# Kernel tuning notes

Measured on AMD Instinct MI355X. Metric: run time of the kernel, lower is better.

Reference implementation:

```python
import jax, jax.numpy as jnp
import numpy as np

COMMITMENT_COST = 0.25
NUM_EMBEDDINGS = 4096
EMBEDDING_DIM = 64


def setup_inputs() -> dict:
    key = jax.random.key(0)
    k1, k2 = jax.random.split(key)
    inputs = jax.random.normal(k1, (32, 32, 32, EMBEDDING_DIM), dtype=jnp.float32)
    # torch init: uniform(-1/K, 1/K)
    lim = 1.0 / NUM_EMBEDDINGS
    embeddings = jax.random.uniform(k2, (NUM_EMBEDDINGS, EMBEDDING_DIM),
                                    dtype=jnp.float32, minval=-lim, maxval=lim)
    return {"inputs": inputs, "embeddings": embeddings}


def reference(inputs, embeddings):
    input_shape = inputs.shape
    flat = inputs.reshape(-1, EMBEDDING_DIM)                      # [N, D]
    x_sq = jnp.sum(flat * flat, axis=1, keepdims=True)            # [N, 1]
    e_sq = jnp.sum(embeddings * embeddings, axis=1)               # [K]
    distances = x_sq - 2.0 * (flat @ embeddings.T) + e_sq[None, :]  # [N, K]
    encoding_indices = jnp.argmin(distances, axis=1)              # [N]
    quantized = embeddings[encoding_indices].reshape(input_shape)  # direct gather == one-hot matmul
    e_latent_loss = jnp.mean((jax.lax.stop_gradient(quantized) - inputs) ** 2)
    q_latent_loss = jnp.mean((quantized - jax.lax.stop_gradient(inputs)) ** 2)
    loss = q_latent_loss + COMMITMENT_COST * e_latent_loss
    # straight-through estimator
    quantized_st = inputs + jax.lax.stop_gradient(quantized - inputs)
    return quantized_st, loss, encoding_indices[:, None]
```

## Files before the change

kernel.cpp:

```cpp
#include <hip/hip_runtime.h>


#define NROWS 32768
#define NK 4096
#define ND 64
#define LOSS_OFF 2097152u
#define IDX_OFF  2097153u
#define EMAX 2.44140625e-4f
#define CAP 48

typedef __attribute__((ext_vector_type(8))) short bf16x8;
typedef __attribute__((ext_vector_type(16))) float f32x16;

__device__ __forceinline__ short f2bf(float f) {
  union { float f; unsigned u; } v; v.f = f;
  unsigned u = v.u;
  return (short)((u + 0x7fffu + ((u >> 16) & 1u)) >> 16);
}
__device__ __forceinline__ unsigned fmap(float f) {
  unsigned u = __float_as_uint(f);
  return (u & 0x80000000u) ? ~u : (u | 0x80000000u);
}
__device__ __forceinline__ float funmap(unsigned m) {
  return __uint_as_float((m & 0x80000000u) ? (m & 0x7fffffffu) : ~m);
}

__global__ __launch_bounds__(256) void k_prep(
    const float* __restrict__ xg, const float* __restrict__ emb,
    bf16x8* __restrict__ ebfT, bf16x8* __restrict__ xbfF,
    float* __restrict__ xsqA, float* __restrict__ marg,
    int* __restrict__ cnt, unsigned* __restrict__ rowbest,
    double* __restrict__ acc) {
  int rt = blockIdx.x, tid = threadIdx.x, l = tid & 63;
  int row = rt * 32 + (l & 31);
  int d0 = (tid >> 6) * 16 + ((l >> 5) << 3);
  {
    const float4* p = reinterpret_cast<const float4*>(xg + (size_t)row * ND + d0);
    float4 u = p[0], v = p[1];
    bf16x8 o;
    o[0] = f2bf(u.x); o[1] = f2bf(u.y); o[2] = f2bf(u.z); o[3] = f2bf(u.w);
    o[4] = f2bf(v.x); o[5] = f2bf(v.y); o[6] = f2bf(v.z); o[7] = f2bf(v.w);
    xbfF[rt * 256 + tid] = o;
  }
  if (rt < 128) {
    int code = rt * 32 + (l & 31);
    const float4* p = reinterpret_cast<const float4*>(emb + (size_t)code * ND + d0);
    float4 u = p[0], v = p[1];
    bf16x8 o;
    o[0] = f2bf(u.x); o[1] = f2bf(u.y); o[2] = f2bf(u.z); o[3] = f2bf(u.w);
    o[4] = f2bf(v.x); o[5] = f2bf(v.y); o[6] = f2bf(v.z); o[7] = f2bf(v.w);
    ebfT[rt * 256 + tid] = o;
  }
  if (tid < 32) {
    int r2 = rt * 32 + tid;
    const float4* xr = reinterpret_cast<const float4*>(xg + (size_t)r2 * ND);
    float xs = 0.f, S = 0.f;
#pragma unroll
    for (int j = 0; j < 16; ++j) {
      float4 w = xr[j];
      xs = fmaf(w.x, w.x, xs); xs = fmaf(w.y, w.y, xs);
      xs = fmaf(w.z, w.z, xs); xs = fmaf(w.w, w.w, xs);
      S += fabsf(w.x) + fabsf(w.y) + fabsf(w.z) + fabsf(w.w);
    }
    xsqA[r2] = xs;
    marg[r2] = EMAX * S * 0.015625f + 1e-5f;
    cnt[r2] = 0;
    rowbest[r2] = 0u;
  }
  if (rt == 0 && tid == 0) acc[0] = 0.0;
}

__global__ __launch_bounds__(512, 8) void k_scan(
    const bf16x8* __restrict__ ebfT, const bf16x8* __restrict__ xbfF,
    const float* __restrict__ marg, unsigned* __restrict__ rowbest,
    int* __restrict__ cnt, uint2* __restrict__ list) {
  __shared__ bf16x8 Alds[2048];
  int bid = blockIdx.x;
  int rb = bid >> 4, cg = bid & 15;
  int tid = threadIdx.x, wv = tid >> 6, l = tid & 63;
  int rt = rb * 8 + wv;
  const bf16x8* xf = xbfF + rt * 256;
  bf16x8 b0 = xf[l], b1 = xf[64 + l], b2 = xf[128 + l], b3 = xf[192 + l];
  const bf16x8* src = ebfT + cg * 2048;
#pragma unroll
  for (int it = 0; it < 4; ++it) Alds[it * 512 + tid] = src[it * 512 + tid];
  __syncthreads();

  int row = rt * 32 + (l & 31);
  float mg = marg[row];
  float tmax[8];
#pragma unroll
  for (int tt = 0; tt < 8; ++tt) {
    bf16x8 a0 = Alds[tt * 256 + l],       a1 = Alds[tt * 256 + 64 + l],
           a2 = Alds[tt * 256 + 128 + l], a3 = Alds[tt * 256 + 192 + l];
    f32x16 acc;
#pragma unroll
    for (int r = 0; r < 16; ++r) acc[r] = 0.f;
    acc = __builtin_amdgcn_mfma_f32_32x32x16_bf16(a0, b0, acc, 0, 0, 0);
    acc = __builtin_amdgcn_mfma_f32_32x32x16_bf16(a1, b1, acc, 0, 0, 0);
    acc = __builtin_amdgcn_mfma_f32_32x32x16_bf16(a2, b2, acc, 0, 0, 0);
    acc = __builtin_amdgcn_mfma_f32_32x32x16_bf16(a3, b3, acc, 0, 0, 0);
    float m = fmaxf(fmaxf(fmaxf(acc[0], acc[1]), fmaxf(acc[2], acc[3])),
                    fmaxf(fmaxf(acc[4], acc[5]), fmaxf(acc[6], acc[7])));
    float m2 = fmaxf(fmaxf(fmaxf(acc[8], acc[9]), fmaxf(acc[10], acc[11])),
                     fmaxf(fmaxf(acc[12], acc[13]), fmaxf(acc[14], acc[15])));
    tmax[tt] = fmaxf(m, m2);
  }
  float rm = tmax[0];
#pragma unroll
  for (int tt = 1; tt < 8; ++tt) rm = fmaxf(rm, tmax[tt]);
  rm = fmaxf(rm, __shfl_xor(rm, 32, 64));
  atomicMax(&rowbest[row], fmap(rm));
  __syncthreads();
  float g = funmap(atomicMax(&rowbest[row], 0u));
  float thr = g - mg;
#pragma unroll
  for (int tt = 0; tt < 8; ++tt) {
    if (__any(tmax[tt] >= thr)) {
      bf16x8 a0 = Alds[tt * 256 + l],       a1 = Alds[tt * 256 + 64 + l],
             a2 = Alds[tt * 256 + 128 + l], a3 = Alds[tt * 256 + 192 + l];
      f32x16 acc;
#pragma unroll
      for (int r = 0; r < 16; ++r) acc[r] = 0.f;
      acc = __builtin_amdgcn_mfma_f32_32x32x16_bf16(a0, b0, acc, 0, 0, 0);
      acc = __builtin_amdgcn_mfma_f32_32x32x16_bf16(a1, b1, acc, 0, 0, 0);
      acc = __builtin_amdgcn_mfma_f32_32x32x16_bf16(a2, b2, acc, 0, 0, 0);
      acc = __builtin_amdgcn_mfma_f32_32x32x16_bf16(a3, b3, acc, 0, 0, 0);
      int kb = cg * 256 + tt * 32 + ((l >> 5) << 2);
#pragma unroll
      for (int r = 0; r < 16; ++r) {
        if (acc[r] >= thr) {
          int k = kb + (r & 3) + ((r >> 2) << 3);
          int slot = atomicAdd(&cnt[row], 1);
          if (slot < CAP)
            list[(size_t)row * CAP + slot] =
                make_uint2((unsigned)k, __float_as_uint(acc[r]));
        }
      }
    }
  }
}

__global__ __launch_bounds__(128) void k_pickout(
    const float* __restrict__ xg, const float* __restrict__ emb,
    const int* __restrict__ cnt, const uint2* __restrict__ list,
    const float* __restrict__ marg, const float* __restrict__ xsqA,
    float* __restrict__ out, double* __restrict__ acc) {
  int row = blockIdx.x * 128 + threadIdx.x;
  int mylane = threadIdx.x & 63;
  float4 X[16];
  const float4* xr = reinterpret_cast<const float4*>(xg + (size_t)row * ND);
#pragma unroll
  for (int j = 0; j < 16; ++j) X[j] = xr[j];
  float xs = xsqA[row], mg = marg[row];
  int c = cnt[row];
  unsigned long long best = ~0ull;

  int cc = c < CAP ? c : CAP;
  const uint2* L = list + (size_t)row * CAP;
  float m = -3.0e38f;
  for (int i = 0; i < cc; ++i) m = fmaxf(m, __uint_as_float(L[i].y));
  float thr = m - mg;
  for (int i = 0; i < cc; ++i) {
    uint2 e = L[i];
    if (__uint_as_float(e.y) >= thr) {
      int k = (int)e.x;
      const float4* er = reinterpret_cast<const float4*>(emb + (size_t)k * ND);
      float q0 = 0.f, q1 = 0.f, q2 = 0.f, q3 = 0.f;
#pragma unroll
      for (int j = 0; j < 16; ++j) {
        float4 E = er[j];
        q0 = fmaf(X[j].x, E.x, q0); q1 = fmaf(X[j].y, E.y, q1);
        q2 = fmaf(X[j].z, E.z, q2); q3 = fmaf(X[j].w, E.w, q3);
      }
      float dot = (q0 + q1) + (q2 + q3);
      float dist = xs - 2.0f * dot;
      unsigned long long key =
          ((unsigned long long)__float_as_uint(dist) << 32) | (unsigned)k;
      best = best < key ? best : key;
    }
  }

  unsigned long long ovf = __ballot(c > CAP);
  while (ovf) {
    int srcl = __ffsll(ovf) - 1;
    ovf &= ovf - 1;
    int orow = __shfl(row, srcl, 64);
    float ys = __shfl(xs, srcl, 64);
    float4 Y[16];
    const float4* yr = reinterpret_cast<const float4*>(xg + (size_t)orow * ND);
#pragma unroll
    for (int j = 0; j < 16; ++j) Y[j] = yr[j];
    unsigned long long wb = ~0ull;
    for (int i = 0; i < 64; ++i) {
      int k = mylane * 64 + i;
      const float4* er = reinterpret_cast<const float4*>(emb + (size_t)k * ND);
      float q0 = 0.f, q1 = 0.f, q2 = 0.f, q3 = 0.f;
#pragma unroll
      for (int j = 0; j < 16; ++j) {
        float4 E = er[j];
        q0 = fmaf(Y[j].x, E.x, q0); q1 = fmaf(Y[j].y, E.y, q1);
        q2 = fmaf(Y[j].z, E.z, q2); q3 = fmaf(Y[j].w, E.w, q3);
      }
      float dot = (q0 + q1) + (q2 + q3);
      float dist = ys - 2.0f * dot;
      unsigned long long key =
          ((unsigned long long)__float_as_uint(dist) << 32) | (unsigned)k;
      wb = wb < key ? wb : key;
    }
#pragma unroll
    for (int off = 32; off > 0; off >>= 1) {
      unsigned long long o = __shfl_xor(wb, off, 64);
      wb = wb < o ? wb : o;
    }
    if (mylane == srcl) best = wb;
  }

  unsigned kwin = ((unsigned)(best & 0xffffffffull)) & 4095u;
  const float4* er = reinterpret_cast<const float4*>(emb + (size_t)kwin * ND);
  float4* op = reinterpret_cast<float4*>(out + (size_t)row * ND);
  float s2 = 0.f;
#pragma unroll
  for (int j = 0; j < 16; ++j) {
    float4 E = er[j];
    float d0 = E.x - X[j].x, d1 = E.y - X[j].y;
    float d2 = E.z - X[j].z, d3 = E.w - X[j].w;
    float4 O = {X[j].x + d0, X[j].y + d1, X[j].z + d2, X[j].w + d3};
    op[j] = O;
    s2 += d0 * d0 + d1 * d1 + d2 * d2 + d3 * d3;
  }
  out[IDX_OFF + (unsigned)row] = (float)kwin;
  double s = (double)s2;
#pragma unroll
  for (int off = 32; off > 0; off >>= 1) s += __shfl_down(s, off, 64);
  if (mylane == 0) atomicAdd(acc, s);
}

__global__ void k_fin(const double* __restrict__ acc, float* __restrict__ out) {
  if (threadIdx.x == 0) out[LOSS_OFF] = (float)(1.25 * acc[0] / 2097152.0);
}

extern "C" void kernel_launch(void* const* d_in, const int* in_sizes, int n_in,
                              void* d_out, int out_size, void* d_ws, size_t ws_size,
                              hipStream_t stream) {
  const float* xg = (const float*)d_in[0];
  const float* emb = (const float*)d_in[1];
  float* out = (float*)d_out;
  char* w = (char*)d_ws;
  bf16x8* ebfT = (bf16x8*)w;
  bf16x8* xbfF = (bf16x8*)(w + 524288);
  float* xsqA = (float*)(w + 4718592);
  float* marg = (float*)(w + 4849664);
  int* cnt    = (int*)(w + 4980736);
  unsigned* rowbest = (unsigned*)(w + 5111808);
  double* acc = (double*)(w + 5373952);
  uint2* list = (uint2*)(w + 5373968);

  k_prep<<<1024, 256, 0, stream>>>(xg, emb, ebfT, xbfF, xsqA, marg, cnt, rowbest, acc);
  k_scan<<<2048, 512, 0, stream>>>(ebfT, xbfF, marg, rowbest, cnt, list);
  k_pickout<<<256, 128, 0, stream>>>(xg, emb, cnt, list, marg, xsqA, out, acc);
  k_fin<<<1, 64, 0, stream>>>(acc, out);
}
```

Before: 131.8 us.

## Single-pass scan with running-max threshold, double-buffered codebook, 8-lane pickout

The two-pass scan, which did a global atomicMax over each row's best score and then recomputed the MFMA tiles, is replaced by a single pass. Each block streams a quarter of the codebook through double-buffered LDS and emits candidates against a per-block running-max threshold. This removes the rowbest buffer, the atomics and the duplicated MFMA work. The pickout kernel now spreads each row over 8 lanes and computes ||x||^2 inline instead of reading it from prep. The running threshold is looser early in the scan, so more candidates may be emitted and rows may overflow CAP more often, which triggers the costly brute-force fallback.

```diff
diff --git a/kernel.cpp b/kernel.cpp
--- a/kernel.cpp
+++ b/kernel.cpp
@@ -17,20 +17,11 @@
   unsigned u = v.u;
   return (short)((u + 0x7fffu + ((u >> 16) & 1u)) >> 16);
 }
-__device__ __forceinline__ unsigned fmap(float f) {
-  unsigned u = __float_as_uint(f);
-  return (u & 0x80000000u) ? ~u : (u | 0x80000000u);
-}
-__device__ __forceinline__ float funmap(unsigned m) {
-  return __uint_as_float((m & 0x80000000u) ? (m & 0x7fffffffu) : ~m);
-}
 
 __global__ __launch_bounds__(256) void k_prep(
     const float* __restrict__ xg, const float* __restrict__ emb,
     bf16x8* __restrict__ ebfT, bf16x8* __restrict__ xbfF,
-    float* __restrict__ xsqA, float* __restrict__ marg,
-    int* __restrict__ cnt, unsigned* __restrict__ rowbest,
-    double* __restrict__ acc) {
+    float* __restrict__ marg, int* __restrict__ cnt, double* __restrict__ acc) {
   int rt = blockIdx.x, tid = threadIdx.x, l = tid & 63;
   int row = rt * 32 + (l & 31);
   int d0 = (tid >> 6) * 16 + ((l >> 5) << 3);
@@ -54,158 +45,159 @@
   if (tid < 32) {
     int r2 = rt * 32 + tid;
     const float4* xr = reinterpret_cast<const float4*>(xg + (size_t)r2 * ND);
-    float xs = 0.f, S = 0.f;
+    float S = 0.f;
 #pragma unroll
     for (int j = 0; j < 16; ++j) {
       float4 w = xr[j];
-      xs = fmaf(w.x, w.x, xs); xs = fmaf(w.y, w.y, xs);
-      xs = fmaf(w.z, w.z, xs); xs = fmaf(w.w, w.w, xs);
       S += fabsf(w.x) + fabsf(w.y) + fabsf(w.z) + fabsf(w.w);
     }
-    xsqA[r2] = xs;
     marg[r2] = EMAX * S * 0.015625f + 1e-5f;
     cnt[r2] = 0;
-    rowbest[r2] = 0u;
   }
   if (rt == 0 && tid == 0) acc[0] = 0.0;
 }
 
-__global__ __launch_bounds__(512, 8) void k_scan(
+__global__ __launch_bounds__(256, 4) void k_scan(
     const bf16x8* __restrict__ ebfT, const bf16x8* __restrict__ xbfF,
-    const float* __restrict__ marg, unsigned* __restrict__ rowbest,
-    int* __restrict__ cnt, uint2* __restrict__ list) {
-  __shared__ bf16x8 Alds[2048];
+    const float* __restrict__ marg, int* __restrict__ cnt,
+    uint2* __restrict__ list) {
+  __shared__ bf16x8 Alds[2][1024];
   int bid = blockIdx.x;
-  int rb = bid >> 4, cg = bid & 15;
+  int rg = bid >> 2, q = bid & 3;
   int tid = threadIdx.x, wv = tid >> 6, l = tid & 63;
-  int rt = rb * 8 + wv;
+  int rt = rg * 4 + wv;
+  int row = rt * 32 + (l & 31);
   const bf16x8* xf = xbfF + rt * 256;
   bf16x8 b0 = xf[l], b1 = xf[64 + l], b2 = xf[128 + l], b3 = xf[192 + l];
-  const bf16x8* src = ebfT + cg * 2048;
-#pragma unroll
-  for (int it = 0; it < 4; ++it) Alds[it * 512 + tid] = src[it * 512 + tid];
+  float mg = marg[row];
+  const bf16x8* src = ebfT + q * 8192;
+
+#pragma unroll
+  for (int it = 0; it < 4; ++it) Alds[0][it * 256 + tid] = src[it * 256 + tid];
   __syncthreads();
 
-  int row = rt * 32 + (l & 31);
-  float mg = marg[row];
-  float tmax[8];
-#pragma unroll
-  for (int tt = 0; tt < 8; ++tt) {
-    bf16x8 a0 = Alds[tt * 256 + l],       a1 = Alds[tt * 256 + 64 + l],
-           a2 = Alds[tt * 256 + 128 + l], a3 = Alds[tt * 256 + 192 + l];
-    f32x16 acc;
-#pragma unroll
-    for (int r = 0; r < 16; ++r) acc[r] = 0.f;
-    acc = __builtin_amdgcn_mfma_f32_32x32x16_bf16(a0, b0, acc, 0, 0, 0);
-    acc = __builtin_amdgcn_mfma_f32_32x32x16_bf16(a1, b1, acc, 0, 0, 0);
-    acc = __builtin_amdgcn_mfma_f32_32x32x16_bf16(a2, b2, acc, 0, 0, 0);
-    acc = __builtin_amdgcn_mfma_f32_32x32x16_bf16(a3, b3, acc, 0, 0, 0);
-    float m = fmaxf(fmaxf(fmaxf(acc[0], acc[1]), fmaxf(acc[2], acc[3])),
-                    fmaxf(fmaxf(acc[4], acc[5]), fmaxf(acc[6], acc[7])));
-    float m2 = fmaxf(fmaxf(fmaxf(acc[8], acc[9]), fmaxf(acc[10], acc[11])),
-                     fmaxf(fmaxf(acc[12], acc[13]), fmaxf(acc[14], acc[15])));
-    tmax[tt] = fmaxf(m, m2);
-  }
-  float rm = tmax[0];
-#pragma unroll
-  for (int tt = 1; tt < 8; ++tt) rm = fmaxf(rm, tmax[tt]);
-  rm = fmaxf(rm, __shfl_xor(rm, 32, 64));
-  atomicMax(&rowbest[row], fmap(rm));
-  __syncthreads();
-  float g = funmap(atomicMax(&rowbest[row], 0u));
-  float thr = g - mg;
-#pragma unroll
-  for (int tt = 0; tt < 8; ++tt) {
-    if (__any(tmax[tt] >= thr)) {
-      bf16x8 a0 = Alds[tt * 256 + l],       a1 = Alds[tt * 256 + 64 + l],
-             a2 = Alds[tt * 256 + 128 + l], a3 = Alds[tt * 256 + 192 + l];
-      f32x16 acc;
-#pragma unroll
-      for (int r = 0; r < 16; ++r) acc[r] = 0.f;
-      acc = __builtin_amdgcn_mfma_f32_32x32x16_bf16(a0, b0, acc, 0, 0, 0);
-      acc = __builtin_amdgcn_mfma_f32_32x32x16_bf16(a1, b1, acc, 0, 0, 0);
-      acc = __builtin_amdgcn_mfma_f32_32x32x16_bf16(a2, b2, acc, 0, 0, 0);
-      acc = __builtin_amdgcn_mfma_f32_32x32x16_bf16(a3, b3, acc, 0, 0, 0);
-      int kb = cg * 256 + tt * 32 + ((l >> 5) << 2);
-#pragma unroll
-      for (int r = 0; r < 16; ++r) {
-        if (acc[r] >= thr) {
-          int k = kb + (r & 3) + ((r >> 2) << 3);
-          int slot = atomicAdd(&cnt[row], 1);
-          if (slot < CAP)
-            list[(size_t)row * CAP + slot] =
-                make_uint2((unsigned)k, __float_as_uint(acc[r]));
+  float rm = -3.0e38f;
+  for (int ch = 0; ch < 8; ++ch) {
+    int cur = ch & 1;
+    bf16x8 p0, p1, p2, p3;
+    if (ch < 7) {
+      const bf16x8* s2 = src + (ch + 1) * 1024;
+      p0 = s2[tid]; p1 = s2[256 + tid]; p2 = s2[512 + tid]; p3 = s2[768 + tid];
+    }
+#pragma unroll
+    for (int tt = 0; tt < 4; ++tt) {
+      const bf16x8* A = &Alds[cur][tt * 256];
+      bf16x8 a0 = A[l], a1 = A[64 + l], a2 = A[128 + l], a3 = A[192 + l];
+      f32x16 ac;
+#pragma unroll
+      for (int r = 0; r < 16; ++r) ac[r] = 0.f;
+      ac = __builtin_amdgcn_mfma_f32_32x32x16_bf16(a0, b0, ac, 0, 0, 0);
+      ac = __builtin_amdgcn_mfma_f32_32x32x16_bf16(a1, b1, ac, 0, 0, 0);
+      ac = __builtin_amdgcn_mfma_f32_32x32x16_bf16(a2, b2, ac, 0, 0, 0);
+      ac = __builtin_amdgcn_mfma_f32_32x32x16_bf16(a3, b3, ac, 0, 0, 0);
+      float m = fmaxf(fmaxf(fmaxf(ac[0], ac[1]), fmaxf(ac[2], ac[3])),
+                      fmaxf(fmaxf(ac[4], ac[5]), fmaxf(ac[6], ac[7])));
+      float m2 = fmaxf(fmaxf(fmaxf(ac[8], ac[9]), fmaxf(ac[10], ac[11])),
+                       fmaxf(fmaxf(ac[12], ac[13]), fmaxf(ac[14], ac[15])));
+      m = fmaxf(m, m2);
+      m = fmaxf(m, __shfl_xor(m, 32, 64));
+      rm = fmaxf(rm, m);
+      float thr = rm - mg;
+      if (__any(m >= thr)) {
+        int kb = q * 1024 + ch * 128 + tt * 32 + ((l >> 5) << 2);
+#pragma unroll
+        for (int r = 0; r < 16; ++r) {
+          if (ac[r] >= thr) {
+            int k = kb + (r & 3) + ((r >> 2) << 3);
+            int slot = atomicAdd(&cnt[row], 1);
+            if (slot < CAP)
+              list[(size_t)row * CAP + slot] =
+                  make_uint2((unsigned)k, __float_as_uint(ac[r]));
+          }
         }
       }
     }
-  }
-}
-
-__global__ __launch_bounds__(128) void k_pickout(
+    if (ch < 7) {
+      bf16x8* D = &Alds[cur ^ 1][0];
+      D[tid] = p0; D[256 + tid] = p1; D[512 + tid] = p2; D[768 + tid] = p3;
+    }
+    __syncthreads();
+  }
+}
+
+__global__ __launch_bounds__(256, 4) void k_pickout(
     const float* __restrict__ xg, const float* __restrict__ emb,
     const int* __restrict__ cnt, const uint2* __restrict__ list,
-    const float* __restrict__ marg, const float* __restrict__ xsqA,
-    float* __restrict__ out, double* __restrict__ acc) {
-  int row = blockIdx.x * 128 + threadIdx.x;
-  int mylane = threadIdx.x & 63;
+    const float* __restrict__ marg, float* __restrict__ out,
+    double* __restrict__ acc) {
+  int tid = threadIdx.x, mylane = tid & 63, wv = tid >> 6;
+  int g = mylane >> 3, j = mylane & 7;
+  int row = blockIdx.x * 32 + wv * 8 + g;
+  const float4* xr = reinterpret_cast<const float4*>(xg + (size_t)row * ND);
   float4 X[16];
-  const float4* xr = reinterpret_cast<const float4*>(xg + (size_t)row * ND);
-#pragma unroll
-  for (int j = 0; j < 16; ++j) X[j] = xr[j];
-  float xs = xsqA[row], mg = marg[row];
+#pragma unroll
+  for (int i = 0; i < 16; ++i) X[i] = xr[i];
+  float xs = 0.f;
+#pragma unroll
+  for (int i = 0; i < 16; ++i) {
+    xs = fmaf(X[i].x, X[i].x, xs); xs = fmaf(X[i].y, X[i].y, xs);
+    xs = fmaf(X[i].z, X[i].z, xs); xs = fmaf(X[i].w, X[i].w, xs);
+  }
+  float mg = marg[row];
   int c = cnt[row];
-  unsigned long long best = ~0ull;
-
   int cc = c < CAP ? c : CAP;
   const uint2* L = list + (size_t)row * CAP;
   float m = -3.0e38f;
-  for (int i = 0; i < cc; ++i) m = fmaxf(m, __uint_as_float(L[i].y));
+  for (int i = j; i < cc; i += 8) m = fmaxf(m, __uint_as_float(L[i].y));
+#pragma unroll
+  for (int off = 4; off > 0; off >>= 1) m = fmaxf(m, __shfl_xor(m, off, 8));
   float thr = m - mg;
-  for (int i = 0; i < cc; ++i) {
+  unsigned long long best = ~0ull;
+  for (int i = j; i < cc; i += 8) {
     uint2 e = L[i];
     if (__uint_as_float(e.y) >= thr) {
-      int k = (int)e.x;
-      const float4* er = reinterpret_cast<const float4*>(emb + (size_t)k * ND);
+      const float4* er = reinterpret_cast<const float4*>(emb + ((size_t)e.x << 6));
       float q0 = 0.f, q1 = 0.f, q2 = 0.f, q3 = 0.f;
 #pragma unroll
-      for (int j = 0; j < 16; ++j) {
-        float4 E = er[j];
-        q0 = fmaf(X[j].x, E.x, q0); q1 = fmaf(X[j].y, E.y, q1);
-        q2 = fmaf(X[j].z, E.z, q2); q3 = fmaf(X[j].w, E.w, q3);
+      for (int t = 0; t < 16; ++t) {
+        float4 E = er[t];
+        q0 = fmaf(X[t].x, E.x, q0); q1 = fmaf(X[t].y, E.y, q1);
+        q2 = fmaf(X[t].z, E.z, q2); q3 = fmaf(X[t].w, E.w, q3);
       }
       float dot = (q0 + q1) + (q2 + q3);
       float dist = xs - 2.0f * dot;
       unsigned long long key =
-          ((unsigned long long)__float_as_uint(dist) << 32) | (unsigned)k;
+          ((unsigned long long)__float_as_uint(dist) << 32) | (unsigned long long)e.x;
       best = best < key ? best : key;
     }
   }
-
-  unsigned long long ovf = __ballot(c > CAP);
+#pragma unroll
+  for (int off = 4; off > 0; off >>= 1) {
+    unsigned long long o = __shfl_xor(best, off, 8);
+    best = best < o ? best : o;
+  }
+  unsigned long long ovf = __ballot(j == 0 && c > CAP);
   while (ovf) {
     int srcl = __ffsll(ovf) - 1;
     ovf &= ovf - 1;
     int orow = __shfl(row, srcl, 64);
     float ys = __shfl(xs, srcl, 64);
-    float4 Y[16];
     const float4* yr = reinterpret_cast<const float4*>(xg + (size_t)orow * ND);
-#pragma unroll
-    for (int j = 0; j < 16; ++j) Y[j] = yr[j];
     unsigned long long wb = ~0ull;
     for (int i = 0; i < 64; ++i) {
       int k = mylane * 64 + i;
-      const float4* er = reinterpret_cast<const float4*>(emb + (size_t)k * ND);
+      const float4* er = reinterpret_cast<const float4*>(emb + ((size_t)k << 6));
       float q0 = 0.f, q1 = 0.f, q2 = 0.f, q3 = 0.f;
 #pragma unroll
-      for (int j = 0; j < 16; ++j) {
-        float4 E = er[j];
-        q0 = fmaf(Y[j].x, E.x, q0); q1 = fmaf(Y[j].y, E.y, q1);
-        q2 = fmaf(Y[j].z, E.z, q2); q3 = fmaf(Y[j].w, E.w, q3);
+      for (int t = 0; t < 16; ++t) {
+        float4 Y = yr[t]; float4 E = er[t];
+        q0 = fmaf(Y.x, E.x, q0); q1 = fmaf(Y.y, E.y, q1);
+        q2 = fmaf(Y.z, E.z, q2); q3 = fmaf(Y.w, E.w, q3);
       }
       float dot = (q0 + q1) + (q2 + q3);
       float dist = ys - 2.0f * dot;
       unsigned long long key =
-          ((unsigned long long)__float_as_uint(dist) << 32) | (unsigned)k;
+          ((unsigned long long)__float_as_uint(dist) << 32) | (unsigned long long)k;
       wb = wb < key ? wb : key;
     }
 #pragma unroll
@@ -213,23 +205,21 @@
       unsigned long long o = __shfl_xor(wb, off, 64);
       wb = wb < o ? wb : o;
     }
-    if (mylane == srcl) best = wb;
-  }
-
+    if ((mylane >> 3) == (srcl >> 3)) best = wb;
+  }
   unsigned kwin = ((unsigned)(best & 0xffffffffull)) & 4095u;
-  const float4* er = reinterpret_cast<const float4*>(emb + (size_t)kwin * ND);
+  const float4* er = reinterpret_cast<const float4*>(emb + ((size_t)kwin << 6));
+  float4 E0 = er[2 * j], E1 = er[2 * j + 1];
+  float4 X0 = X[2 * j], X1 = X[2 * j + 1];
+  float d0 = E0.x - X0.x, d1 = E0.y - X0.y, d2 = E0.z - X0.z, d3 = E0.w - X0.w;
+  float d4 = E1.x - X1.x, d5 = E1.y - X1.y, d6 = E1.z - X1.z, d7 = E1.w - X1.w;
+  float4 O0 = {X0.x + d0, X0.y + d1, X0.z + d2, X0.w + d3};
+  float4 O1 = {X1.x + d4, X1.y + d5, X1.z + d6, X1.w + d7};
   float4* op = reinterpret_cast<float4*>(out + (size_t)row * ND);
-  float s2 = 0.f;
-#pragma unroll
-  for (int j = 0; j < 16; ++j) {
-    float4 E = er[j];
-    float d0 = E.x - X[j].x, d1 = E.y - X[j].y;
-    float d2 = E.z - X[j].z, d3 = E.w - X[j].w;
-    float4 O = {X[j].x + d0, X[j].y + d1, X[j].z + d2, X[j].w + d3};
-    op[j] = O;
-    s2 += d0 * d0 + d1 * d1 + d2 * d2 + d3 * d3;
-  }
-  out[IDX_OFF + (unsigned)row] = (float)kwin;
+  op[2 * j] = O0; op[2 * j + 1] = O1;
+  if (j == 0) out[IDX_OFF + (unsigned)row] = (float)kwin;
+  float s2 = d0 * d0 + d1 * d1 + d2 * d2 + d3 * d3 +
+             d4 * d4 + d5 * d5 + d6 * d6 + d7 * d7;
   double s = (double)s2;
 #pragma unroll
   for (int off = 32; off > 0; off >>= 1) s += __shfl_down(s, off, 64);
@@ -249,15 +239,13 @@
   char* w = (char*)d_ws;
   bf16x8* ebfT = (bf16x8*)w;
   bf16x8* xbfF = (bf16x8*)(w + 524288);
-  float* xsqA = (float*)(w + 4718592);
-  float* marg = (float*)(w + 4849664);
-  int* cnt    = (int*)(w + 4980736);
-  unsigned* rowbest = (unsigned*)(w + 5111808);
-  double* acc = (double*)(w + 5373952);
-  uint2* list = (uint2*)(w + 5373968);
-
-  k_prep<<<1024, 256, 0, stream>>>(xg, emb, ebfT, xbfF, xsqA, marg, cnt, rowbest, acc);
-  k_scan<<<2048, 512, 0, stream>>>(ebfT, xbfF, marg, rowbest, cnt, list);
-  k_pickout<<<256, 128, 0, stream>>>(xg, emb, cnt, list, marg, xsqA, out, acc);
+  float* marg  = (float*)(w + 4718592);
+  int* cnt     = (int*)(w + 4849664);
+  double* acc  = (double*)(w + 4980736);
+  uint2* list  = (uint2*)(w + 4980752);
+
+  k_prep<<<1024, 256, 0, stream>>>(xg, emb, ebfT, xbfF, marg, cnt, acc);
+  k_scan<<<1024, 256, 0, stream>>>(ebfT, xbfF, marg, cnt, list);
+  k_pickout<<<1024, 256, 0, stream>>>(xg, emb, cnt, list, marg, out, acc);
   k_fin<<<1, 64, 0, stream>>>(acc, out);
 }
```

After: 336.2 us. +155.1%, slower.

## Drop cross-block rowbest atomics and split each pickout row across four lanes

Applied to the files above, without the earlier changes.

The scan kernel no longer publishes a global per-row maximum through atomics and a block barrier. Each block now thresholds against the maximum from its own 256-code slice, so more candidates get written and the per-row list overflows into the brute-force fallback more often. The prep kernel stops re-reading rows to compute squared norms; it builds the abs-sum margin through a shared-memory reduction instead. The pickout kernel spreads each row over four lanes that share candidate evaluation and output writes, and it computes the squared norm itself rather than storing it in a workspace buffer.

```diff
diff --git a/kernel.cpp b/kernel.cpp
--- a/kernel.cpp
+++ b/kernel.cpp
@@ -17,20 +17,12 @@
   unsigned u = v.u;
   return (short)((u + 0x7fffu + ((u >> 16) & 1u)) >> 16);
 }
-__device__ __forceinline__ unsigned fmap(float f) {
-  unsigned u = __float_as_uint(f);
-  return (u & 0x80000000u) ? ~u : (u | 0x80000000u);
-}
-__device__ __forceinline__ float funmap(unsigned m) {
-  return __uint_as_float((m & 0x80000000u) ? (m & 0x7fffffffu) : ~m);
-}
 
 __global__ __launch_bounds__(256) void k_prep(
     const float* __restrict__ xg, const float* __restrict__ emb,
     bf16x8* __restrict__ ebfT, bf16x8* __restrict__ xbfF,
-    float* __restrict__ xsqA, float* __restrict__ marg,
-    int* __restrict__ cnt, unsigned* __restrict__ rowbest,
-    double* __restrict__ acc) {
+    float* __restrict__ marg, int* __restrict__ cnt, double* __restrict__ acc) {
+  __shared__ float Sp[256];
   int rt = blockIdx.x, tid = threadIdx.x, l = tid & 63;
   int row = rt * 32 + (l & 31);
   int d0 = (tid >> 6) * 16 + ((l >> 5) << 3);
@@ -41,6 +33,8 @@
     o[0] = f2bf(u.x); o[1] = f2bf(u.y); o[2] = f2bf(u.z); o[3] = f2bf(u.w);
     o[4] = f2bf(v.x); o[5] = f2bf(v.y); o[6] = f2bf(v.z); o[7] = f2bf(v.w);
     xbfF[rt * 256 + tid] = o;
+    Sp[tid] = fabsf(u.x) + fabsf(u.y) + fabsf(u.z) + fabsf(u.w) +
+              fabsf(v.x) + fabsf(v.y) + fabsf(v.z) + fabsf(v.w);
   }
   if (rt < 128) {
     int code = rt * 32 + (l & 31);
@@ -51,29 +45,22 @@
     o[4] = f2bf(v.x); o[5] = f2bf(v.y); o[6] = f2bf(v.z); o[7] = f2bf(v.w);
     ebfT[rt * 256 + tid] = o;
   }
+  __syncthreads();
   if (tid < 32) {
+    float S = 0.f;
+#pragma unroll
+    for (int i = 0; i < 8; ++i) S += Sp[tid + 32 * i];
     int r2 = rt * 32 + tid;
-    const float4* xr = reinterpret_cast<const float4*>(xg + (size_t)r2 * ND);
-    float xs = 0.f, S = 0.f;
-#pragma unroll
-    for (int j = 0; j < 16; ++j) {
-      float4 w = xr[j];
-      xs = fmaf(w.x, w.x, xs); xs = fmaf(w.y, w.y, xs);
-      xs = fmaf(w.z, w.z, xs); xs = fmaf(w.w, w.w, xs);
-      S += fabsf(w.x) + fabsf(w.y) + fabsf(w.z) + fabsf(w.w);
-    }
-    xsqA[r2] = xs;
     marg[r2] = EMAX * S * 0.015625f + 1e-5f;
     cnt[r2] = 0;
-    rowbest[r2] = 0u;
   }
   if (rt == 0 && tid == 0) acc[0] = 0.0;
 }
 
 __global__ __launch_bounds__(512, 8) void k_scan(
     const bf16x8* __restrict__ ebfT, const bf16x8* __restrict__ xbfF,
-    const float* __restrict__ marg, unsigned* __restrict__ rowbest,
-    int* __restrict__ cnt, uint2* __restrict__ list) {
+    const float* __restrict__ marg, int* __restrict__ cnt,
+    uint2* __restrict__ list) {
   __shared__ bf16x8 Alds[2048];
   int bid = blockIdx.x;
   int rb = bid >> 4, cg = bid & 15;
@@ -110,10 +97,7 @@
 #pragma unroll
   for (int tt = 1; tt < 8; ++tt) rm = fmaxf(rm, tmax[tt]);
   rm = fmaxf(rm, __shfl_xor(rm, 32, 64));
-  atomicMax(&rowbest[row], fmap(rm));
-  __syncthreads();
-  float g = funmap(atomicMax(&rowbest[row], 0u));
-  float thr = g - mg;
+  float thr = rm - mg;
 #pragma unroll
   for (int tt = 0; tt < 8; ++tt) {
     if (__any(tmax[tt] >= thr)) {
@@ -141,71 +125,77 @@
   }
 }
 
-__global__ __launch_bounds__(128) void k_pickout(
+__global__ __launch_bounds__(256) void k_pickout(
     const float* __restrict__ xg, const float* __restrict__ emb,
     const int* __restrict__ cnt, const uint2* __restrict__ list,
-    const float* __restrict__ marg, const float* __restrict__ xsqA,
-    float* __restrict__ out, double* __restrict__ acc) {
-  int row = blockIdx.x * 128 + threadIdx.x;
-  int mylane = threadIdx.x & 63;
-  float4 X[16];
+    const float* __restrict__ marg, float* __restrict__ out,
+    double* __restrict__ acc) {
+  int tid = threadIdx.x, mylane = tid & 63;
+  int gid = blockIdx.x * 256 + tid;
+  int row = gid >> 2, j = gid & 3;
   const float4* xr = reinterpret_cast<const float4*>(xg + (size_t)row * ND);
-#pragma unroll
-  for (int j = 0; j < 16; ++j) X[j] = xr[j];
-  float xs = xsqA[row], mg = marg[row];
+  float xs = 0.f;
+#pragma unroll
+  for (int t = 0; t < 16; ++t) {
+    float4 v = xr[t];
+    xs = fmaf(v.x, v.x, xs); xs = fmaf(v.y, v.y, xs);
+    xs = fmaf(v.z, v.z, xs); xs = fmaf(v.w, v.w, xs);
+  }
+  float mg = marg[row];
   int c = cnt[row];
-  unsigned long long best = ~0ull;
-
   int cc = c < CAP ? c : CAP;
   const uint2* L = list + (size_t)row * CAP;
   float m = -3.0e38f;
-  for (int i = 0; i < cc; ++i) m = fmaxf(m, __uint_as_float(L[i].y));
+  for (int i = j; i < cc; i += 4) m = fmaxf(m, __uint_as_float(L[i].y));
+#pragma unroll
+  for (int off = 2; off > 0; off >>= 1) m = fmaxf(m, __shfl_xor(m, off, 4));
   float thr = m - mg;
-  for (int i = 0; i < cc; ++i) {
+  unsigned long long best = ~0ull;
+  for (int i = j; i < cc; i += 4) {
     uint2 e = L[i];
     if (__uint_as_float(e.y) >= thr) {
-      int k = (int)e.x;
-      const float4* er = reinterpret_cast<const float4*>(emb + (size_t)k * ND);
+      const float4* er = reinterpret_cast<const float4*>(emb + ((size_t)e.x << 6));
       float q0 = 0.f, q1 = 0.f, q2 = 0.f, q3 = 0.f;
 #pragma unroll
-      for (int j = 0; j < 16; ++j) {
-        float4 E = er[j];
-        q0 = fmaf(X[j].x, E.x, q0); q1 = fmaf(X[j].y, E.y, q1);
-        q2 = fmaf(X[j].z, E.z, q2); q3 = fmaf(X[j].w, E.w, q3);
+      for (int t = 0; t < 16; ++t) {
+        float4 X = xr[t], E = er[t];
+        q0 = fmaf(X.x, E.x, q0); q1 = fmaf(X.y, E.y, q1);
+        q2 = fmaf(X.z, E.z, q2); q3 = fmaf(X.w, E.w, q3);
       }
       float dot = (q0 + q1) + (q2 + q3);
       float dist = xs - 2.0f * dot;
       unsigned long long key =
-          ((unsigned long long)__float_as_uint(dist) << 32) | (unsigned)k;
+          ((unsigned long long)__float_as_uint(dist) << 32) | (unsigned long long)e.x;
       best = best < key ? best : key;
     }
   }
-
-  unsigned long long ovf = __ballot(c > CAP);
+#pragma unroll
+  for (int off = 2; off > 0; off >>= 1) {
+    unsigned long long o = __shfl_xor(best, off, 4);
+    best = best < o ? best : o;
+  }
+  unsigned long long ovf = __ballot(j == 0 && c > CAP);
   while (ovf) {
     int srcl = __ffsll(ovf) - 1;
     ovf &= ovf - 1;
     int orow = __shfl(row, srcl, 64);
     float ys = __shfl(xs, srcl, 64);
-    float4 Y[16];
     const float4* yr = reinterpret_cast<const float4*>(xg + (size_t)orow * ND);
-#pragma unroll
-    for (int j = 0; j < 16; ++j) Y[j] = yr[j];
     unsigned long long wb = ~0ull;
     for (int i = 0; i < 64; ++i) {
       int k = mylane * 64 + i;
-      const float4* er = reinterpret_cast<const float4*>(emb + (size_t)k * ND);
+      const float4* er = reinterpret_cast<const float4*>(emb + ((size_t)k << 6));
       float q0 = 0.f, q1 = 0.f, q2 = 0.f, q3 = 0.f;
 #pragma unroll
-      for (int j = 0; j < 16; ++j) {
-        float4 E = er[j];
-        q0 = fmaf(Y[j].x, E.x, q0); q1 = fmaf(Y[j].y, E.y, q1);
-        q2 = fmaf(Y[j].z, E.z, q2); q3 = fmaf(Y[j].w, E.w, q3);
+      for (int t = 0; t < 16; ++t) {
+        float4 Y = yr[t], E = er[t];
+        q0 = fmaf(Y.x, E.x, q0); q1 = fmaf(Y.y, E.y, q1);
+        q2 = fmaf(Y.z, E.z, q2); q3 = fmaf(Y.w, E.w, q3);
       }
       float dot = (q0 + q1) + (q2 + q3);
       float dist = ys - 2.0f * dot;
       unsigned long long key =
-          ((unsigned long long)__float_as_uint(dist) << 32) | (unsigned)k;
+          ((unsigned long long)__float_as_uint(dist) << 32) | (unsigned long long)k;
       wb = wb < key ? wb : key;
     }
 #pragma unroll
@@ -213,23 +203,21 @@
       unsigned long long o = __shfl_xor(wb, off, 64);
       wb = wb < o ? wb : o;
     }
-    if (mylane == srcl) best = wb;
-  }
-
+    if ((mylane >> 2) == (srcl >> 2)) best = wb;
+  }
   unsigned kwin = ((unsigned)(best & 0xffffffffull)) & 4095u;
-  const float4* er = reinterpret_cast<const float4*>(emb + (size_t)kwin * ND);
-  float4* op = reinterpret_cast<float4*>(out + (size_t)row * ND);
+  const float4* er = reinterpret_cast<const float4*>(emb + ((size_t)kwin << 6));
+  float4* op = reinterpret_cast<float4*>(out) + (size_t)row * 16;
   float s2 = 0.f;
 #pragma unroll
-  for (int j = 0; j < 16; ++j) {
-    float4 E = er[j];
-    float d0 = E.x - X[j].x, d1 = E.y - X[j].y;
-    float d2 = E.z - X[j].z, d3 = E.w - X[j].w;
-    float4 O = {X[j].x + d0, X[j].y + d1, X[j].z + d2, X[j].w + d3};
-    op[j] = O;
+  for (int t = 0; t < 4; ++t) {
+    float4 X = xr[4 * j + t], E = er[4 * j + t];
+    float d0 = E.x - X.x, d1 = E.y - X.y, d2 = E.z - X.z, d3 = E.w - X.w;
+    float4 O = {X.x + d0, X.y + d1, X.z + d2, X.w + d3};
+    op[4 * j + t] = O;
     s2 += d0 * d0 + d1 * d1 + d2 * d2 + d3 * d3;
   }
-  out[IDX_OFF + (unsigned)row] = (float)kwin;
+  if (j == 0) out[IDX_OFF + (unsigned)row] = (float)kwin;
   double s = (double)s2;
 #pragma unroll
   for (int off = 32; off > 0; off >>= 1) s += __shfl_down(s, off, 64);
@@ -249,15 +237,13 @@
   char* w = (char*)d_ws;
   bf16x8* ebfT = (bf16x8*)w;
   bf16x8* xbfF = (bf16x8*)(w + 524288);
-  float* xsqA = (float*)(w + 4718592);
-  float* marg = (float*)(w + 4849664);
-  int* cnt    = (int*)(w + 4980736);
-  unsigned* rowbest = (unsigned*)(w + 5111808);
-  double* acc = (double*)(w + 5373952);
-  uint2* list = (uint2*)(w + 5373968);
-
-  k_prep<<<1024, 256, 0, stream>>>(xg, emb, ebfT, xbfF, xsqA, marg, cnt, rowbest, acc);
-  k_scan<<<2048, 512, 0, stream>>>(ebfT, xbfF, marg, rowbest, cnt, list);
-  k_pickout<<<256, 128, 0, stream>>>(xg, emb, cnt, list, marg, xsqA, out, acc);
+  float* marg  = (float*)(w + 4718592);
+  int* cnt     = (int*)(w + 4849664);
+  double* acc  = (double*)(w + 4980736);
+  uint2* list  = (uint2*)(w + 4980752);
+
+  k_prep<<<1024, 256, 0, stream>>>(xg, emb, ebfT, xbfF, marg, cnt, acc);
+  k_scan<<<2048, 512, 0, stream>>>(ebfT, xbfF, marg, cnt, list);
+  k_pickout<<<512, 256, 0, stream>>>(xg, emb, cnt, list, marg, out, acc);
   k_fin<<<1, 64, 0, stream>>>(acc, out);
 }
```

After: 292.7 us. 122% more time.
